# Optimization experiments

Measured on AMD Instinct MI355X. Metric: run time of the kernel, lower is better.

Reference implementation:

```python
import jax, jax.numpy as jnp
import numpy as np

B, T, C, H = 4, 2048, 2048, 16
HD = C // H  # head_size = 128
EPS = 1e-5


def layernorm(x, g, b):
    mu = jnp.mean(x, axis=-1, keepdims=True)
    var = jnp.var(x, axis=-1, keepdims=True)
    return (x - mu) * jax.lax.rsqrt(var + EPS) * g + b


def setup_inputs() -> dict:
    key = jax.random.key(0)
    ks = jax.random.split(key, 12)
    s_attn = 1.0 / np.sqrt(C)
    s_ffn1 = 1.0 / np.sqrt(C)
    s_ffn2 = 1.0 / np.sqrt(4 * C)
    return {
        "x": jax.random.normal(ks[0], (B, T, C), jnp.float32),
        "Wq": jax.random.normal(ks[1], (H, C, HD), jnp.float32) * s_attn,
        "Wk": jax.random.normal(ks[2], (H, C, HD), jnp.float32) * s_attn,
        "Wv": jax.random.normal(ks[3], (H, C, HD), jnp.float32) * s_attn,
        "Wp": jax.random.normal(ks[4], (C, C), jnp.float32) * s_attn,
        "bp": jnp.zeros((C,), jnp.float32),
        "W1": jax.random.normal(ks[5], (C, 4 * C), jnp.float32) * s_ffn1,
        "b1": jnp.zeros((4 * C,), jnp.float32),
        "W2": jax.random.normal(ks[6], (4 * C, C), jnp.float32) * s_ffn2,
        "b2": jnp.zeros((C,), jnp.float32),
        "g1": jnp.ones((C,), jnp.float32),
        "beta1": jnp.zeros((C,), jnp.float32),
        "g2": jnp.ones((C,), jnp.float32),
        "beta2": jnp.zeros((C,), jnp.float32),
    }


def reference(x, Wq, Wk, Wv, Wp, bp, W1, b1, W2, b2, g1, beta1, g2, beta2):
    # --- attention sublayer (pre-LN, causal) ---
    h = layernorm(x, g1, beta1)
    q = jnp.einsum("btc,hcd->bhtd", h, Wq)
    k = jnp.einsum("bsc,hcd->bhsd", h, Wk)
    v = jnp.einsum("bsc,hcd->bhsd", h, Wv)
    scores = jnp.einsum("bhtd,bhsd->bhts", q, k) / jnp.sqrt(jnp.asarray(HD, x.dtype))
    causal = jnp.tril(jnp.ones((T, T), bool))
    scores = jnp.where(causal, scores, jnp.asarray(-jnp.inf, x.dtype))
    w = jax.nn.softmax(scores, axis=-1)  # dropout = identity (eval mode)
    o = jnp.einsum("bhts,bhsd->bhtd", w, v)
    o = o.transpose(0, 2, 1, 3).reshape(B, T, C)  # concat heads
    x = x + o @ Wp + bp
    # --- feed-forward sublayer ---
    h2 = layernorm(x, g2, beta2)
    f = jax.nn.gelu(h2 @ W1 + b1, approximate=False)
    x = x + f @ W2 + b2
    return x
```

## Files before the change

kernel.cpp:

```cpp
#include <hip/hip_runtime.h>
#include <math.h>

#define B_ 4
#define T_ 2048
#define C_ 2048
#define H_ 16
#define HD_ 128

typedef __attribute__((ext_vector_type(8))) short short8;
typedef __attribute__((ext_vector_type(4))) float f32x4;
typedef unsigned short u16;
typedef unsigned int u32;

__device__ __forceinline__ u16 f2bf(float f) {
  union { float f; unsigned u; } v; v.f = f;
  unsigned r = v.u + 0x7FFFu + ((v.u >> 16) & 1u);
  return (u16)(r >> 16);
}

__device__ __forceinline__ void gld16(const void* g, void* l) {
  __builtin_amdgcn_global_load_lds(
      (__attribute__((address_space(1))) void*)(void*)g,
      (__attribute__((address_space(3))) void*)l, 16, 0, 0);
}

__global__ __launch_bounds__(256) void tconv(const float* __restrict__ in,
                                             u16* __restrict__ out,
                                             int K, int N,
                                             long inBS, long outBS) {
  __shared__ float tile[32][33];
  const float* inb = in + (long)blockIdx.z * inBS;
  u16* outb = out + (long)blockIdx.z * outBS;
  int k0 = blockIdx.x << 5, n0 = blockIdx.y << 5;
  int t = threadIdx.x;
  {
    int kk = t >> 3, nn = (t & 7) << 2;
    float4 v = *(const float4*)(inb + (long)(k0 + kk) * N + n0 + nn);
    tile[kk][nn + 0] = v.x; tile[kk][nn + 1] = v.y;
    tile[kk][nn + 2] = v.z; tile[kk][nn + 3] = v.w;
  }
  __syncthreads();
  {
    int nn = t >> 3, kk = (t & 7) << 2;
    ushort4 o;
    o.x = f2bf(tile[kk + 0][nn]); o.y = f2bf(tile[kk + 1][nn]);
    o.z = f2bf(tile[kk + 2][nn]); o.w = f2bf(tile[kk + 3][nn]);
    *(ushort4*)(outb + (long)(n0 + nn) * K + k0 + kk) = o;
  }
}

__global__ __launch_bounds__(256) void ln_rows(const float* __restrict__ x,
                                               const float* __restrict__ gam,
                                               const float* __restrict__ bet,
                                               u16* __restrict__ out) {
  int row = blockIdx.x;
  const float* xr = x + (size_t)row * C_;
  int t = threadIdx.x;
  float4 v0 = *(const float4*)(xr + t * 8);
  float4 v1 = *(const float4*)(xr + t * 8 + 4);
  float s = v0.x + v0.y + v0.z + v0.w + v1.x + v1.y + v1.z + v1.w;
  float ss = v0.x * v0.x + v0.y * v0.y + v0.z * v0.z + v0.w * v0.w +
             v1.x * v1.x + v1.y * v1.y + v1.z * v1.z + v1.w * v1.w;
  for (int d = 32; d > 0; d >>= 1) {
    s += __shfl_down(s, d);
    ss += __shfl_down(ss, d);
  }
  __shared__ float red[8];
  int wv = t >> 6;
  if ((t & 63) == 0) { red[wv] = s; red[4 + wv] = ss; }
  __syncthreads();
  s = red[0] + red[1] + red[2] + red[3];
  ss = red[4] + red[5] + red[6] + red[7];
  float mu = s * (1.0f / C_);
  float var = ss * (1.0f / C_) - mu * mu;
  float rs = rsqrtf(var + 1e-5f);
  int c = t * 8;
  float vv[8] = {v0.x, v0.y, v0.z, v0.w, v1.x, v1.y, v1.z, v1.w};
  ushort4 o0, o1;
  o0.x = f2bf((vv[0] - mu) * rs * gam[c + 0] + bet[c + 0]);
  o0.y = f2bf((vv[1] - mu) * rs * gam[c + 1] + bet[c + 1]);
  o0.z = f2bf((vv[2] - mu) * rs * gam[c + 2] + bet[c + 2]);
  o0.w = f2bf((vv[3] - mu) * rs * gam[c + 3] + bet[c + 3]);
  o1.x = f2bf((vv[4] - mu) * rs * gam[c + 4] + bet[c + 4]);
  o1.y = f2bf((vv[5] - mu) * rs * gam[c + 5] + bet[c + 5]);
  o1.z = f2bf((vv[6] - mu) * rs * gam[c + 6] + bet[c + 6]);
  o1.w = f2bf((vv[7] - mu) * rs * gam[c + 7] + bet[c + 7]);
  *(ushort4*)(out + (size_t)row * C_ + c) = o0;
  *(ushort4*)(out + (size_t)row * C_ + c + 4) = o1;
}

template <int EPI>
__global__ __launch_bounds__(512, 2) void gemm256(
    const u16* __restrict__ A, const u16* __restrict__ BT,
    int M, int N, int K, int lda, int ldb,
    u16* __restrict__ oq, u16* __restrict__ ok, u16* __restrict__ ovt,
    float* __restrict__ of32, const float* __restrict__ resid,
    const float* __restrict__ bias, u16* __restrict__ obf, int addBias) {
  extern __shared__ char smem[];
  int nbx = N >> 8;
  int nwg = gridDim.x;
  int flat = blockIdx.x;
  int sw = (flat & 7) * (nwg >> 3) + (flat >> 3);
  int bx = sw % nbx, by = sw / nbx;
  int m0 = by << 8, n0 = bx << 8;
  int tid = threadIdx.x;
  int lane = tid & 63, wave = tid >> 6;
  int wm = wave >> 2, wn = wave & 3;
  int l15 = lane & 15, l16 = lane >> 4;
  int nt = K >> 6;

  f32x4 acc[8][4] = {};
  short8 af[4][2], bf[4][2];

  auto stage = [&](int b, int r, int k0) {
    int row = (r & 3) * 64 + (tid >> 3);
    int lslot = (tid & 7) ^ (row & 7);
    char* dst = smem + ((r < 4) ? 0 : 65536) + b * 32768 + (r & 3) * 8192 + tid * 16;
    const u16* src = ((r < 4) ? (A + (long)(m0 + row) * lda)
                              : (BT + (long)(n0 + row) * ldb)) +
                     k0 + lslot * 8;
    gld16(src, dst);
  };
  auto ldA = [&](int cur, int mf, int kk) {
    int row = wm * 128 + mf * 16 + l15;
    int slot = (kk * 4 + l16) ^ (row & 7);
    return *(const short8*)(smem + cur * 32768 + row * 128 + slot * 16);
  };
  auto ldB = [&](int cur, int nf, int kk) {
    int row = wn * 64 + nf * 16 + l15;
    int slot = (kk * 4 + l16) ^ (row & 7);
    return *(const short8*)(smem + 65536 + cur * 32768 + row * 128 + slot * 16);
  };

#pragma unroll
  for (int r = 0; r < 8; ++r) stage(0, r, 0);

  for (int t = 0; t < nt; ++t) {
    int cur = t & 1, nxt = cur ^ 1;
    bool more = (t + 1) < nt;
    int k1 = (t + 1) << 6;
    if (more) {
      stage(nxt, 0, k1); stage(nxt, 1, k1); stage(nxt, 2, k1);
      asm volatile("s_waitcnt vmcnt(3)" ::: "memory");
    } else {
      asm volatile("s_waitcnt vmcnt(0)" ::: "memory");
    }
    __builtin_amdgcn_s_barrier();
#pragma unroll
    for (int mq = 0; mq < 4; ++mq)
#pragma unroll
      for (int kk = 0; kk < 2; ++kk) af[mq][kk] = ldA(cur, mq, kk);
#pragma unroll
    for (int nq = 0; nq < 2; ++nq)
#pragma unroll
      for (int kk = 0; kk < 2; ++kk) bf[nq][kk] = ldB(cur, nq, kk);
    if (more) { stage(nxt, 3, k1); stage(nxt, 4, k1); stage(nxt, 5, k1); }
    __builtin_amdgcn_s_barrier();
    asm volatile("s_waitcnt lgkmcnt(0)" ::: "memory");
    __builtin_amdgcn_s_setprio(1);
#pragma unroll
    for (int mq = 0; mq < 4; ++mq)
#pragma unroll
      for (int nq = 0; nq < 2; ++nq)
#pragma unroll
        for (int kk = 0; kk < 2; ++kk)
          acc[mq][nq] = __builtin_amdgcn_mfma_f32_16x16x32_bf16(
              af[mq][kk], bf[nq][kk], acc[mq][nq], 0, 0, 0);
    __builtin_amdgcn_s_setprio(0);
    __builtin_amdgcn_s_barrier();
#pragma unroll
    for (int nq = 2; nq < 4; ++nq)
#pragma unroll
      for (int kk = 0; kk < 2; ++kk) bf[nq][kk] = ldB(cur, nq, kk);
    if (more) { stage(nxt, 6, k1); stage(nxt, 7, k1); }
    __builtin_amdgcn_s_barrier();
    asm volatile("s_waitcnt lgkmcnt(0)" ::: "memory");
    __builtin_amdgcn_s_setprio(1);
#pragma unroll
    for (int mq = 0; mq < 4; ++mq)
#pragma unroll
      for (int nq = 2; nq < 4; ++nq)
#pragma unroll
        for (int kk = 0; kk < 2; ++kk)
          acc[mq][nq] = __builtin_amdgcn_mfma_f32_16x16x32_bf16(
              af[mq][kk], bf[nq][kk], acc[mq][nq], 0, 0, 0);
    __builtin_amdgcn_s_setprio(0);
    __builtin_amdgcn_s_barrier();
#pragma unroll
    for (int mq = 0; mq < 4; ++mq)
#pragma unroll
      for (int kk = 0; kk < 2; ++kk) af[mq][kk] = ldA(cur, 4 + mq, kk);
    __builtin_amdgcn_s_barrier();
    asm volatile("s_waitcnt lgkmcnt(0)" ::: "memory");
    __builtin_amdgcn_s_setprio(1);
#pragma unroll
    for (int mq = 0; mq < 4; ++mq)
#pragma unroll
      for (int nq = 0; nq < 2; ++nq)
#pragma unroll
        for (int kk = 0; kk < 2; ++kk)
          acc[4 + mq][nq] = __builtin_amdgcn_mfma_f32_16x16x32_bf16(
              af[mq][kk], bf[nq][kk], acc[4 + mq][nq], 0, 0, 0);
    __builtin_amdgcn_s_setprio(0);
    __builtin_amdgcn_s_barrier();
    __builtin_amdgcn_s_setprio(1);
#pragma unroll
    for (int mq = 0; mq < 4; ++mq)
#pragma unroll
      for (int nq = 2; nq < 4; ++nq)
#pragma unroll
        for (int kk = 0; kk < 2; ++kk)
          acc[4 + mq][nq] = __builtin_amdgcn_mfma_f32_16x16x32_bf16(
              af[mq][kk], bf[nq][kk], acc[4 + mq][nq], 0, 0, 0);
    __builtin_amdgcn_s_setprio(0);
    __builtin_amdgcn_s_barrier();
  }

#pragma unroll
  for (int mf = 0; mf < 8; ++mf) {
#pragma unroll
    for (int nf = 0; nf < 4; ++nf) {
      int rowf = m0 + wm * 128 + mf * 16 + l16 * 4;
      int col = n0 + wn * 64 + nf * 16 + l15;
      if constexpr (EPI == 0) {
        int seg = col >> 11, cn = col & 2047;
        int hh = cn >> 7, dd = cn & 127;
        int bb = rowf >> 11, t0 = rowf & 2047;
        if (seg == 2) {
          ushort4 o;
          o.x = f2bf(acc[mf][nf][0]); o.y = f2bf(acc[mf][nf][1]);
          o.z = f2bf(acc[mf][nf][2]); o.w = f2bf(acc[mf][nf][3]);
          *(ushort4*)(ovt + ((long)(bb * H_ + hh) * HD_ + dd) * T_ + t0) = o;
        } else {
          u16* dst = (seg == 0) ? oq : ok;
#pragma unroll
          for (int r = 0; r < 4; ++r)
            dst[((long)(bb * H_ + hh) * T_ + t0 + r) * HD_ + dd] =
                f2bf(acc[mf][nf][r]);
        }
      } else if constexpr (EPI == 1) {
#pragma unroll
        for (int r = 0; r < 4; ++r) {
          long idx = (long)(rowf + r) * N + col;
          of32[idx] = resid[idx] + bias[col] + acc[mf][nf][r];
        }
      } else if constexpr (EPI == 2) {
#pragma unroll
        for (int r = 0; r < 4; ++r) {
          float v = acc[mf][nf][r] + bias[col];
          float g = 0.5f * v * (1.0f + erff(v * 0.70710678118654752f));
          obf[(long)(rowf + r) * N + col] = f2bf(g);
        }
      } else {
#pragma unroll
        for (int r = 0; r < 4; ++r) {
          long idx = (long)(rowf + r) * N + col;
          float v = acc[mf][nf][r];
          if (addBias) v += bias[col];
          of32[idx] += v;
        }
      }
    }
  }
}

__global__ __launch_bounds__(256) void attn_fwd(const u16* __restrict__ q,
                                                const u16* __restrict__ k,
                                                const u16* __restrict__ vt,
                                                u16* __restrict__ o) {
  __shared__ u16 Ks[64 * 128];
  __shared__ u16 Vs[128 * 64];
  __shared__ u16 Ps[4][16 * 64];
  int bid = blockIdx.x;
  int bh = bid & 63;
  int qb = 31 - (bid >> 6);
  int q0 = qb << 6;
  int tid = threadIdx.x, lane = tid & 63, wave = tid >> 6;
  int l15 = lane & 15, l16 = lane >> 4;
  int wq0 = q0 + wave * 16;

  short8 qf[4];
#pragma unroll
  for (int kk = 0; kk < 4; ++kk)
    qf[kk] = *(const short8*)(q + ((long)bh * T_ + wq0 + l15) * HD_ +
                              kk * 32 + l16 * 8);

  f32x4 accO[8] = {};
  float m_r[4], l_r[4];
#pragma unroll
  for (int r = 0; r < 4; ++r) { m_r[r] = -INFINITY; l_r[r] = 0.f; }
  const float sc = 0.08838834764831845f * 1.4426950408889634f;

  int nt = qb + 1;
  int off0 = wave * 4096 + lane * 16;

  int4 kreg[4], vreg[4];
  auto regload = [&](int t) {
    int s0 = t << 6;
#pragma unroll
    for (int it = 0; it < 4; ++it) {
      int off = off0 + it * 1024;
      int krow = off >> 8;
      kreg[it] = *(const int4*)((const char*)(k + ((long)bh * T_ + s0 + krow) * HD_) +
                                (off & 255));
      int dd = off >> 7;
      vreg[it] = *(const int4*)((const char*)(vt + ((long)bh * HD_ + dd) * T_ + s0) +
                                (off & 127));
    }
  };
  auto dswrite = [&]() {
#pragma unroll
    for (int it = 0; it < 4; ++it) {
      int off = off0 + it * 1024;
      int krow = off >> 8;
      *(int4*)((char*)Ks + (off ^ ((krow & 7) << 4))) = kreg[it];
      int dd = off >> 7;
      *(int4*)((char*)Vs + (off ^ ((dd & 7) << 4))) = vreg[it];
    }
  };

  regload(0);
  dswrite();
  __syncthreads();

  for (int t = 0; t < nt; ++t) {
    int s0 = t << 6;
    bool more = (t + 1 < nt);
    if (more) regload(t + 1);

    if (s0 <= wq0 + 15) {
      bool needmask = (s0 + 63 > wq0);
      f32x4 S[4];
#pragma unroll
      for (int sb = 0; sb < 4; ++sb) {
        f32x4 s = {};
#pragma unroll
        for (int kk = 0; kk < 4; ++kk) {
          int srow = sb * 16 + l15;
          int kb = srow * 256 + (((kk * 4 + l16) ^ (srow & 7)) << 4);
          short8 kf = *(const short8*)((const char*)Ks + kb);
          s = __builtin_amdgcn_mfma_f32_16x16x32_bf16(qf[kk], kf, s, 0, 0, 0);
        }
        S[sb] = s;
      }
      float mxl[4];
      bool growL = false;
#pragma unroll
      for (int r = 0; r < 4; ++r) {
        int tt = wq0 + 4 * l16 + r;
        float mx = -INFINITY;
#pragma unroll
        for (int sb = 0; sb < 4; ++sb) {
          float v = S[sb][r] * sc;
          if (needmask && (s0 + sb * 16 + l15 > tt)) v = -INFINITY;
          S[sb][r] = v;
          mx = fmaxf(mx, v);
        }
        mxl[r] = mx;
        growL = growL || (mx > m_r[r] + 8.0f);
      }
      bool anyg = __any(growL);
      float al[4];
      if (anyg) {
#pragma unroll
        for (int r = 0; r < 4; ++r) {
          float mx = mxl[r];
          mx = fmaxf(mx, __shfl_xor(mx, 1));
          mx = fmaxf(mx, __shfl_xor(mx, 2));
          mx = fmaxf(mx, __shfl_xor(mx, 4));
          mx = fmaxf(mx, __shfl_xor(mx, 8));
          float mo = m_r[r];
          float mn = fmaxf(mo, mx);
          al[r] = exp2f(mo - mn);
          m_r[r] = mn;
        }
      } else {
#pragma unroll
        for (int r = 0; r < 4; ++r) al[r] = 1.0f;
      }
#pragma unroll
      for (int r = 0; r < 4; ++r) {
        float mn = m_r[r];
        int prow = 4 * l16 + r;
        float rs = 0.f;
#pragma unroll
        for (int sb = 0; sb < 4; ++sb) {
          float p = exp2f(S[sb][r] - mn);
          rs += p;
          int pb = (prow * 128 + (sb * 16 + l15) * 2) ^ ((prow & 7) << 4);
          *(u16*)((char*)Ps[wave] + pb) = f2bf(p);
        }
        rs += __shfl_xor(rs, 1);
        rs += __shfl_xor(rs, 2);
        rs += __shfl_xor(rs, 4);
        rs += __shfl_xor(rs, 8);
        l_r[r] = l_r[r] * al[r] + rs;
      }
      if (anyg) {
#pragma unroll
        for (int db = 0; db < 8; ++db)
#pragma unroll
          for (int r = 0; r < 4; ++r) accO[db][r] *= al[r];
      }
      short8 pf[2];
#pragma unroll
      for (int st = 0; st < 2; ++st) {
        int prow = l15;
        int pb = (prow * 128 + (st * 4 + l16) * 16) ^ ((prow & 7) << 4);
        pf[st] = *(const short8*)((const char*)Ps[wave] + pb);
      }
#pragma unroll
      for (int db = 0; db < 8; ++db) {
#pragma unroll
        for (int st = 0; st < 2; ++st) {
          int vrow = db * 16 + l15;
          int vb = (vrow * 128 + (st * 4 + l16) * 16) ^ ((vrow & 7) << 4);
          short8 vf = *(const short8*)((const char*)Vs + vb);
          accO[db] = __builtin_amdgcn_mfma_f32_16x16x32_bf16(pf[st], vf,
                                                             accO[db], 0, 0, 0);
        }
      }
    }
    __syncthreads();
    if (more) {
      dswrite();
      __syncthreads();
    }
  }

  int bb = bh >> 4, hh = bh & 15;
  float inv[4];
#pragma unroll
  for (int r = 0; r < 4; ++r) inv[r] = 1.0f / l_r[r];
#pragma unroll
  for (int db = 0; db < 8; ++db)
#pragma unroll
    for (int r = 0; r < 4; ++r) {
      int tt = wq0 + 4 * l16 + r;
      o[((long)bb * T_ + tt) * C_ + hh * HD_ + db * 16 + l15] =
          f2bf(accO[db][r] * inv[r]);
    }
}

extern "C" void kernel_launch(void* const* d_in, const int* in_sizes, int n_in,
                              void* d_out, int out_size, void* d_ws, size_t ws_size,
                              hipStream_t stream) {
  (void)in_sizes; (void)n_in; (void)out_size; (void)ws_size;
  const float* x   = (const float*)d_in[0];
  const float* Wq  = (const float*)d_in[1];
  const float* Wk  = (const float*)d_in[2];
  const float* Wv  = (const float*)d_in[3];
  const float* Wp  = (const float*)d_in[4];
  const float* bp  = (const float*)d_in[5];
  const float* W1  = (const float*)d_in[6];
  const float* b1  = (const float*)d_in[7];
  const float* W2  = (const float*)d_in[8];
  const float* b2  = (const float*)d_in[9];
  const float* g1  = (const float*)d_in[10];
  const float* be1 = (const float*)d_in[11];
  const float* g2  = (const float*)d_in[12];
  const float* be2 = (const float*)d_in[13];
  float* out = (float*)d_out;

  (void)hipFuncSetAttribute((const void*)gemm256<0>,
                            hipFuncAttributeMaxDynamicSharedMemorySize, 131072);
  (void)hipFuncSetAttribute((const void*)gemm256<1>,
                            hipFuncAttributeMaxDynamicSharedMemorySize, 131072);
  (void)hipFuncSetAttribute((const void*)gemm256<2>,
                            hipFuncAttributeMaxDynamicSharedMemorySize, 131072);
  (void)hipFuncSetAttribute((const void*)gemm256<3>,
                            hipFuncAttributeMaxDynamicSharedMemorySize, 131072);

  char* ws = (char*)d_ws;
  size_t off = 0;
  auto alloc = [&](size_t n) {
    void* p = ws + off;
    off += (n + 255) & ~(size_t)255;
    return p;
  };
  u16* wqkvT = (u16*)alloc((size_t)6144 * 2048 * 2);
  u16* wpT   = (u16*)alloc((size_t)2048 * 2048 * 2);
  u16* w1T   = (u16*)alloc((size_t)8192 * 2048 * 2);
  u16* w2T   = (u16*)alloc((size_t)2048 * 8192 * 2);
  u16* hb    = (u16*)alloc((size_t)8192 * 2048 * 2);
  u16* qbuf  = (u16*)alloc((size_t)8192 * 2048 * 2);
  u16* kbuf  = (u16*)alloc((size_t)8192 * 2048 * 2);
  u16* vtbuf = (u16*)alloc((size_t)8192 * 2048 * 2);
  u16* ob = hb;
  u16* fb = qbuf;

  tconv<<<dim3(64, 4, 16), 256, 0, stream>>>(Wq, wqkvT, 2048, 128,
                                             (long)2048 * 128, (long)128 * 2048);
  tconv<<<dim3(64, 4, 16), 256, 0, stream>>>(Wk, wqkvT + (size_t)2048 * 2048, 2048, 128,
                                             (long)2048 * 128, (long)128 * 2048);
  tconv<<<dim3(64, 4, 16), 256, 0, stream>>>(Wv, wqkvT + (size_t)4096 * 2048, 2048, 128,
                                             (long)2048 * 128, (long)128 * 2048);
  tconv<<<dim3(64, 64, 1), 256, 0, stream>>>(Wp, wpT, 2048, 2048, 0, 0);
  tconv<<<dim3(64, 256, 1), 256, 0, stream>>>(W1, w1T, 2048, 8192, 0, 0);
  tconv<<<dim3(256, 64, 1), 256, 0, stream>>>(W2, w2T, 8192, 2048, 0, 0);

  ln_rows<<<8192, 256, 0, stream>>>(x, g1, be1, hb);
  gemm256<0><<<768, 512, 131072, stream>>>(hb, wqkvT, 8192, 6144, 2048, 2048, 2048,
                                           qbuf, kbuf, vtbuf, nullptr, nullptr,
                                           nullptr, nullptr, 0);
  attn_fwd<<<2048, 256, 0, stream>>>(qbuf, kbuf, vtbuf, ob);
  gemm256<1><<<256, 512, 131072, stream>>>(ob, wpT, 8192, 2048, 2048, 2048, 2048,
                                           nullptr, nullptr, nullptr, out, x, bp,
                                           nullptr, 0);

  ln_rows<<<8192, 256, 0, stream>>>(out, g2, be2, hb);
  for (int c = 0; c < 2; ++c) {
    gemm256<2><<<512, 512, 131072, stream>>>(hb, w1T + (size_t)c * 4096 * 2048,
                                             8192, 4096, 2048, 2048, 2048,
                                             nullptr, nullptr, nullptr, nullptr,
                                             nullptr, b1 + c * 4096, fb, 0);
    gemm256<3><<<256, 512, 131072, stream>>>(fb, w2T + (size_t)c * 4096,
                                             8192, 2048, 4096, 4096, 8192,
                                             nullptr, nullptr, nullptr, out,
                                             nullptr, b2, nullptr, c == 0 ? 1 : 0);
  }
}
```

Baseline: 1.313 ms.

## Double-buffer attention K/V tiles with direct global-to-LDS loads

The attention kernel no longer stages K/V tiles through registers followed by a separate LDS write and second barrier. It now issues global_load_lds into a double-buffered LDS region (swizzle applied on the global source address), so the next tile loads while the current one is computed, with one barrier per iteration. This removes register pressure and one synchronisation per tile. In exchange, LDS use per block grows to 72KB of dynamic shared memory, which may reduce how many blocks fit on each CU.

Result: faster. 1.142 ms (-13.0%).

```diff
diff --git a/kernel.cpp b/kernel.cpp
--- a/kernel.cpp
+++ b/kernel.cpp
@@ -268,9 +268,7 @@
                                                 const u16* __restrict__ k,
                                                 const u16* __restrict__ vt,
                                                 u16* __restrict__ o) {
-  __shared__ u16 Ks[64 * 128];
-  __shared__ u16 Vs[128 * 64];
-  __shared__ u16 Ps[4][16 * 64];
+  extern __shared__ char asmem[];
   int bid = blockIdx.x;
   int bh = bid & 63;
   int qb = 31 - (bid >> 6);
@@ -278,6 +276,9 @@
   int tid = threadIdx.x, lane = tid & 63, wave = tid >> 6;
   int l15 = lane & 15, l16 = lane >> 4;
   int wq0 = q0 + wave * 16;
+  const u16* kbase = k + (long)bh * T_ * HD_;
+  const u16* vbase = vt + (long)bh * HD_ * T_;
+  char* Psw = asmem + 65536 + wave * 2048;
 
   short8 qf[4];
 #pragma unroll
@@ -292,43 +293,36 @@
   const float sc = 0.08838834764831845f * 1.4426950408889634f;
 
   int nt = qb + 1;
-  int off0 = wave * 4096 + lane * 16;
-
-  int4 kreg[4], vreg[4];
-  auto regload = [&](int t) {
+
+  auto stage = [&](int b, int t) {
     int s0 = t << 6;
-#pragma unroll
-    for (int it = 0; it < 4; ++it) {
-      int off = off0 + it * 1024;
+    char* Kd = asmem + b * 16384;
+    char* Vd = asmem + 32768 + b * 16384;
+#pragma unroll
+    for (int r = 0; r < 4; ++r) {
+      int off = r * 4096 + tid * 16;
       int krow = off >> 8;
-      kreg[it] = *(const int4*)((const char*)(k + ((long)bh * T_ + s0 + krow) * HD_) +
-                                (off & 255));
+      int kslot = (tid & 15) ^ (krow & 7);
+      gld16(kbase + (long)(s0 + krow) * HD_ + kslot * 8, Kd + off);
       int dd = off >> 7;
-      vreg[it] = *(const int4*)((const char*)(vt + ((long)bh * HD_ + dd) * T_ + s0) +
-                                (off & 127));
+      int vslot = (tid & 7) ^ (dd & 7);
+      gld16(vbase + (long)dd * T_ + s0 + vslot * 8, Vd + off);
     }
   };
-  auto dswrite = [&]() {
-#pragma unroll
-    for (int it = 0; it < 4; ++it) {
-      int off = off0 + it * 1024;
-      int krow = off >> 8;
-      *(int4*)((char*)Ks + (off ^ ((krow & 7) << 4))) = kreg[it];
-      int dd = off >> 7;
-      *(int4*)((char*)Vs + (off ^ ((dd & 7) << 4))) = vreg[it];
-    }
-  };
-
-  regload(0);
-  dswrite();
+
+  stage(0, 0);
+  asm volatile("s_waitcnt vmcnt(0)" ::: "memory");
   __syncthreads();
 
   for (int t = 0; t < nt; ++t) {
     int s0 = t << 6;
+    int cur = t & 1;
     bool more = (t + 1 < nt);
-    if (more) regload(t + 1);
+    if (more) stage(cur ^ 1, t + 1);
 
     if (s0 <= wq0 + 15) {
+      const char* Kc = asmem + cur * 16384;
+      const char* Vc = asmem + 32768 + cur * 16384;
       bool needmask = (s0 + 63 > wq0);
       f32x4 S[4];
 #pragma unroll
@@ -338,7 +332,7 @@
         for (int kk = 0; kk < 4; ++kk) {
           int srow = sb * 16 + l15;
           int kb = srow * 256 + (((kk * 4 + l16) ^ (srow & 7)) << 4);
-          short8 kf = *(const short8*)((const char*)Ks + kb);
+          short8 kf = *(const short8*)(Kc + kb);
           s = __builtin_amdgcn_mfma_f32_16x16x32_bf16(qf[kk], kf, s, 0, 0, 0);
         }
         S[sb] = s;
@@ -388,7 +382,7 @@
           float p = exp2f(S[sb][r] - mn);
           rs += p;
           int pb = (prow * 128 + (sb * 16 + l15) * 2) ^ ((prow & 7) << 4);
-          *(u16*)((char*)Ps[wave] + pb) = f2bf(p);
+          *(u16*)(Psw + pb) = f2bf(p);
         }
         rs += __shfl_xor(rs, 1);
         rs += __shfl_xor(rs, 2);
@@ -407,7 +401,7 @@
       for (int st = 0; st < 2; ++st) {
         int prow = l15;
         int pb = (prow * 128 + (st * 4 + l16) * 16) ^ ((prow & 7) << 4);
-        pf[st] = *(const short8*)((const char*)Ps[wave] + pb);
+        pf[st] = *(const short8*)(Psw + pb);
       }
 #pragma unroll
       for (int db = 0; db < 8; ++db) {
@@ -415,17 +409,14 @@
         for (int st = 0; st < 2; ++st) {
           int vrow = db * 16 + l15;
           int vb = (vrow * 128 + (st * 4 + l16) * 16) ^ ((vrow & 7) << 4);
-          short8 vf = *(const short8*)((const char*)Vs + vb);
+          short8 vf = *(const short8*)(Vc + vb);
           accO[db] = __builtin_amdgcn_mfma_f32_16x16x32_bf16(pf[st], vf,
                                                              accO[db], 0, 0, 0);
         }
       }
     }
+    if (more) asm volatile("s_waitcnt vmcnt(0)" ::: "memory");
     __syncthreads();
-    if (more) {
-      dswrite();
-      __syncthreads();
-    }
   }
 
   int bb = bh >> 4, hh = bh & 15;
@@ -470,6 +461,8 @@
                             hipFuncAttributeMaxDynamicSharedMemorySize, 131072);
   (void)hipFuncSetAttribute((const void*)gemm256<3>,
                             hipFuncAttributeMaxDynamicSharedMemorySize, 131072);
+  (void)hipFuncSetAttribute((const void*)attn_fwd,
+                            hipFuncAttributeMaxDynamicSharedMemorySize, 73728);
 
   char* ws = (char*)d_ws;
   size_t off = 0;
@@ -503,7 +496,7 @@
   gemm256<0><<<768, 512, 131072, stream>>>(hb, wqkvT, 8192, 6144, 2048, 2048, 2048,
                                            qbuf, kbuf, vtbuf, nullptr, nullptr,
                                            nullptr, nullptr, 0);
-  attn_fwd<<<2048, 256, 0, stream>>>(qbuf, kbuf, vtbuf, ob);
+  attn_fwd<<<2048, 256, 73728, stream>>>(qbuf, kbuf, vtbuf, ob);
   gemm256<1><<<256, 512, 131072, stream>>>(ob, wpT, 8192, 2048, 2048, 2048, 2048,
                                            nullptr, nullptr, nullptr, out, x, bp,
                                            nullptr, 0);
```
